# Kernel optimization log

Hardware: AMD Instinct MI355X
Metric: run time of the kernel (lower is better)

The kernel has to match this reference:

```python
import jax, jax.numpy as jnp
import numpy as np

NUM_WIRES = 4
N_LAYERS = 2
HIDDEN = 64
NUM_CLASSES = 10
B = 4096


def _ry(state, theta, wire):
    # state: (N,2,2,2,2); theta: scalar or (N,)
    st = jnp.moveaxis(state, wire + 1, 1)
    c = jnp.reshape(jnp.cos(theta / 2), (-1, 1, 1, 1))
    s = jnp.reshape(jnp.sin(theta / 2), (-1, 1, 1, 1))
    n0 = c * st[:, 0] - s * st[:, 1]
    n1 = s * st[:, 0] + c * st[:, 1]
    st = jnp.stack([n0, n1], axis=1)
    return jnp.moveaxis(st, 1, wire + 1)


def _cnot(state, ctrl, tgt):
    st = jnp.moveaxis(state, (ctrl + 1, tgt + 1), (1, 2))  # (N,2,2,2,2)
    st = jnp.stack([st[:, 0], st[:, 1, ::-1]], axis=1)
    return jnp.moveaxis(st, (1, 2), (ctrl + 1, tgt + 1))


def _zexp(state, wire):
    p = state * state  # real statevector -> probabilities
    axes = tuple(a for a in range(1, 5) if a != wire + 1)
    marg = p.sum(axes)  # (N,2)
    return marg[:, 0] - marg[:, 1]


def quantum_layer(angles, vparams):
    # angles: (N,4) data rotation angles; vparams: (2,4)
    N = angles.shape[0]
    state = jnp.zeros((N, 2, 2, 2, 2), angles.dtype).at[:, 0, 0, 0, 0].set(1.0)
    for w in range(NUM_WIRES):
        state = _ry(state, angles[:, w], w)
    for l in range(N_LAYERS):
        for w in range(NUM_WIRES):
            state = _ry(state, vparams[l, w], w)
        state = _cnot(state, 0, 1)
        state = _cnot(state, 1, 2)
        state = _cnot(state, 2, 3)
    return jnp.stack([_zexp(state, w) for w in range(NUM_WIRES)], axis=1)  # (N,4)


def setup_inputs() -> dict:
    key = jax.random.key(0)
    ks = jax.random.split(key, 8)
    x = jax.random.uniform(ks[0], (B, 28, 28), dtype=jnp.float32)
    vparams = jax.random.normal(ks[1], (N_LAYERS, NUM_WIRES), dtype=jnp.float32)
    w1 = jax.random.normal(ks[2], (HIDDEN, NUM_WIRES), dtype=jnp.float32) * 0.5
    b1 = jnp.zeros((HIDDEN,), jnp.float32)
    w2 = jax.random.normal(ks[3], (1, HIDDEN), dtype=jnp.float32) * 0.125
    b2 = jnp.zeros((1,), jnp.float32)
    W = jax.random.normal(ks[4], (NUM_CLASSES, NUM_WIRES * 14 * 14), dtype=jnp.float32) * 0.03
    b = jnp.zeros((NUM_CLASSES,), jnp.float32)
    return {"x": x, "vparams": vparams, "w1": w1, "b1": b1, "w2": w2, "b2": b2, "W": W, "b": b}


def reference(x, vparams, w1, b1, w2, b2, W, b):
    Bx = x.shape[0]
    # 2x2 stride-2 patches, order [(r,c),(r,c+1),(r+1,c),(r+1,c+1)], patches row-major
    patches = x.reshape(Bx, 14, 2, 14, 2).transpose(0, 1, 3, 2, 4).reshape(Bx, 196, 4)
    meas = quantum_layer(patches.reshape(-1, 4), vparams).reshape(Bx, 196, 4)
    h = jax.nn.relu(jnp.einsum('bpn,hn->bph', meas, w1) + b1)
    scores = (jnp.einsum('bph,oh->bpo', h, w2) + b2)[..., 0]  # (B,196)
    attn = jax.nn.softmax(scores, axis=1)[..., None]
    weighted = meas * attn
    flat = weighted.reshape(Bx, -1)  # (B,784)
    logits = flat @ W.T + b
    return jax.nn.log_softmax(logits, axis=-1)
```

## Files before the change

kernel.cpp:

```cpp
#include <hip/hip_runtime.h>
#include <math.h>

#define NP 196
#define NC 10

template<int CTRL>
__device__ __forceinline__ float dpp_sum_step(float x) {
    int t = __builtin_amdgcn_update_dpp(0, __float_as_int(x), CTRL, 0xf, 0xf, false);
    return x + __int_as_float(t);
}
__device__ __forceinline__ float row16_sum(float x) {
    x = dpp_sum_step<0x111>(x);
    x = dpp_sum_step<0x112>(x);
    x = dpp_sum_step<0x114>(x);
    x = dpp_sum_step<0x118>(x);
    return x;
}
__device__ __forceinline__ float bcast_lane(float x, int lane) {
    return __int_as_float(__builtin_amdgcn_readlane(__float_as_int(x), lane));
}

__global__ __launch_bounds__(256, 4) void quanv_fused(
    const float* __restrict__ x,
    const float* __restrict__ vparams,
    const float* __restrict__ w1,
    const float* __restrict__ b1,
    const float* __restrict__ w2,
    const float* __restrict__ b2,
    const float* __restrict__ W,
    const float* __restrict__ bias,
    float* __restrict__ out)
{
    __shared__ float s_part[11][16];

    const int tid  = threadIdx.x;
    const int b    = blockIdx.x;
    const int lane = tid & 63;
    const int wv   = tid >> 6;
    const int pt   = (tid < NP) ? tid : NP - 1;

    const int pr = pt / 14;
    const int pc = pt - pr * 14;
    const float* px = x + (size_t)b * 784 + (2 * pr) * 28 + 2 * pc;
    const float2 ra = *(const float2*)px;
    const float2 rb = *(const float2*)(px + 28);

    float cw[4], sw[4];
    __sincosf((ra.x + vparams[0]) * 0.5f, &sw[0], &cw[0]);
    __sincosf((ra.y + vparams[1]) * 0.5f, &sw[1], &cw[1]);
    __sincosf((rb.x + vparams[2]) * 0.5f, &sw[2], &cw[2]);
    __sincosf((rb.y + vparams[3]) * 0.5f, &sw[3], &cw[3]);

    float t[4] = {cw[0]*cw[1], cw[0]*sw[1], sw[0]*cw[1], sw[0]*sw[1]};
    float u[4] = {cw[2]*cw[3], cw[2]*sw[3], sw[2]*cw[3], sw[2]*sw[3]};
    float v[16];
    #pragma unroll
    for (int i = 0; i < 16; i++) v[i] = t[i >> 2] * u[i & 3];

    #pragma unroll
    for (int i = 0; i < 16; i++)
        if ((i & 8) && !(i & 4)) { const float tm = v[i]; v[i] = v[i | 4]; v[i | 4] = tm; }
    #pragma unroll
    for (int i = 0; i < 16; i++)
        if ((i & 4) && !(i & 2)) { const float tm = v[i]; v[i] = v[i | 2]; v[i | 2] = tm; }
    #pragma unroll
    for (int i = 0; i < 16; i++)
        if ((i & 2) && !(i & 1)) { const float tm = v[i]; v[i] = v[i | 1]; v[i | 1] = tm; }

    #pragma unroll
    for (int w = 0; w < 4; w++) {
        float c, s;
        __sincosf(vparams[4 + w] * 0.5f, &s, &c);
        const int m = 8 >> w;
        #pragma unroll
        for (int i = 0; i < 16; i++) {
            if ((i & m) == 0) {
                const float v0 = v[i], v1 = v[i | m];
                v[i]     = c * v0 - s * v1;
                v[i | m] = s * v0 + c * v1;
            }
        }
    }
    #pragma unroll
    for (int i = 0; i < 16; i++)
        if ((i & 8) && !(i & 4)) { const float tm = v[i]; v[i] = v[i | 4]; v[i | 4] = tm; }
    #pragma unroll
    for (int i = 0; i < 16; i++)
        if ((i & 4) && !(i & 2)) { const float tm = v[i]; v[i] = v[i | 2]; v[i | 2] = tm; }
    #pragma unroll
    for (int i = 0; i < 16; i++)
        if ((i & 2) && !(i & 1)) { const float tm = v[i]; v[i] = v[i | 1]; v[i | 1] = tm; }

    float p[16];
    #pragma unroll
    for (int i = 0; i < 16; i++) p[i] = v[i] * v[i];
    float e8[8], d8[8];
    #pragma unroll
    for (int j = 0; j < 8; j++) { e8[j] = p[2*j] + p[2*j+1]; d8[j] = p[2*j] - p[2*j+1]; }
    const float meas3 = ((d8[0]+d8[1]) + (d8[2]+d8[3])) + ((d8[4]+d8[5]) + (d8[6]+d8[7]));
    float f4[4], g4[4];
    #pragma unroll
    for (int k = 0; k < 4; k++) { f4[k] = e8[2*k] + e8[2*k+1]; g4[k] = e8[2*k] - e8[2*k+1]; }
    const float meas2 = (g4[0]+g4[1]) + (g4[2]+g4[3]);
    const float meas1 = (f4[0]-f4[1]) + (f4[2]-f4[3]);
    const float meas0 = (f4[0]+f4[1]) - (f4[2]+f4[3]);

    float sc0 = b2[0], sc1 = 0.f, sc2 = 0.f, sc3 = 0.f;
    #pragma unroll
    for (int j = 0; j < 64; j += 4) {
        float h0 = fmaf(w1[j*4 +  0], meas0, fmaf(w1[j*4 +  1], meas1,
                   fmaf(w1[j*4 +  2], meas2, fmaf(w1[j*4 +  3], meas3, b1[j]))));
        float h1 = fmaf(w1[j*4 +  4], meas0, fmaf(w1[j*4 +  5], meas1,
                   fmaf(w1[j*4 +  6], meas2, fmaf(w1[j*4 +  7], meas3, b1[j+1]))));
        float h2 = fmaf(w1[j*4 +  8], meas0, fmaf(w1[j*4 +  9], meas1,
                   fmaf(w1[j*4 + 10], meas2, fmaf(w1[j*4 + 11], meas3, b1[j+2]))));
        float h3 = fmaf(w1[j*4 + 12], meas0, fmaf(w1[j*4 + 13], meas1,
                   fmaf(w1[j*4 + 14], meas2, fmaf(w1[j*4 + 15], meas3, b1[j+3]))));
        sc0 = fmaf(w2[j],     fmaxf(h0, 0.f), sc0);
        sc1 = fmaf(w2[j + 1], fmaxf(h1, 0.f), sc1);
        sc2 = fmaf(w2[j + 2], fmaxf(h2, 0.f), sc2);
        sc3 = fmaf(w2[j + 3], fmaxf(h3, 0.f), sc3);
    }
    const float sc = (sc0 + sc1) + (sc2 + sc3);

    const float e = (tid < NP) ? __expf(sc) : 0.f;
    const float wm0 = e * meas0, wm1 = e * meas1;
    const float wm2 = e * meas2, wm3 = e * meas3;

    float r[11];
    #pragma unroll
    for (int o = 0; o < NC; o++) {
        const float4 Wv = *(const float4*)(W + o * 784 + pt * 4);
        r[o] = fmaf(wm0, Wv.x, fmaf(wm1, Wv.y, fmaf(wm2, Wv.z, wm3 * Wv.w)));
    }
    r[10] = e;

    #pragma unroll
    for (int i = 0; i < 11; i++) r[i] = row16_sum(r[i]);
    if ((lane & 15) == 15) {
        const int row = (wv << 2) | (lane >> 4);
        #pragma unroll
        for (int i = 0; i < 11; i++) s_part[i][row] = r[i];
    }
    __syncthreads();

    if (wv == 0) {
        float tot = 0.f;
        if (lane < 11) {
            const float4* q = (const float4*)s_part[lane];
            const float4 a = q[0], c = q[1], d = q[2], g = q[3];
            tot = (((a.x+a.y) + (a.z+a.w)) + ((c.x+c.y) + (c.z+c.w)))
                + (((d.x+d.y) + (d.z+d.w)) + ((g.x+g.y) + (g.z+g.w)));
        }
        const float esum = bcast_lane(tot, 10);
        const float rinv = __builtin_amdgcn_rcpf(esum);
        float logit = 0.f, ee = 0.f;
        if (lane < NC) {
            logit = fmaf(tot, rinv, bias[lane]);
            ee = __expf(logit);
        }
        const float ls = row16_sum(ee);
        const float lse = bcast_lane(ls, 15);
        if (lane < NC)
            out[(size_t)b * NC + lane] = logit - __logf(lse);
    }
}

extern "C" void kernel_launch(void* const* d_in, const int* in_sizes, int n_in,
                              void* d_out, int out_size, void* d_ws, size_t ws_size,
                              hipStream_t stream) {
    const float* x       = (const float*)d_in[0];
    const float* vparams = (const float*)d_in[1];
    const float* w1      = (const float*)d_in[2];
    const float* b1      = (const float*)d_in[3];
    const float* w2      = (const float*)d_in[4];
    const float* b2      = (const float*)d_in[5];
    const float* W       = (const float*)d_in[6];
    const float* bias    = (const float*)d_in[7];
    float* out           = (float*)d_out;

    const int B = in_sizes[0] / 784;
    quanv_fused<<<B, 256, 0, stream>>>(x, vparams, w1, b1, w2, b2, W, bias, out);
}
```

Before: 90.81 us.

## Map one image per wavefront with lanes looping over patches

Each wavefront now handles a whole image instead of each block handling one image with one patch per thread. Each lane simulates up to four patches in two passes, and the per-class reductions become pure wavefront DPP/readlane sums, so shared memory and the block barrier are gone. This also removes idle threads: 60 of 256 threads sat unused before, and now only the padded tail of the last pass is wasted. In exchange each lane does more serial work and holds more live registers, and W is reloaded per image per wave.

```diff
diff --git a/kernel.cpp b/kernel.cpp
--- a/kernel.cpp
+++ b/kernel.cpp
@@ -18,6 +18,98 @@
 }
 __device__ __forceinline__ float bcast_lane(float x, int lane) {
     return __int_as_float(__builtin_amdgcn_readlane(__float_as_int(x), lane));
+}
+__device__ __forceinline__ float wave_sum(float x) {
+    x = row16_sum(x);
+    x = dpp_sum_step<0x142>(x);
+    x = dpp_sum_step<0x143>(x);
+    return bcast_lane(x, 63);
+}
+
+__device__ __forceinline__ void patch_sim(
+    const float* __restrict__ xb, int p,
+    float vp0, float vp1, float vp2, float vp3,
+    const float* __restrict__ c1, const float* __restrict__ s1,
+    const float* __restrict__ w1, const float* __restrict__ b1,
+    const float* __restrict__ w2, float b2v,
+    float& m0, float& m1, float& m2, float& m3, float& sc)
+{
+    const int pr = p / 14;
+    const int pc = p - pr * 14;
+    const float* px = xb + (2 * pr) * 28 + 2 * pc;
+    const float2 ra = *(const float2*)px;
+    const float2 rb = *(const float2*)(px + 28);
+
+    float cw[4], sw[4];
+    __sincosf((ra.x + vp0) * 0.5f, &sw[0], &cw[0]);
+    __sincosf((ra.y + vp1) * 0.5f, &sw[1], &cw[1]);
+    __sincosf((rb.x + vp2) * 0.5f, &sw[2], &cw[2]);
+    __sincosf((rb.y + vp3) * 0.5f, &sw[3], &cw[3]);
+
+    float t[4] = {cw[0]*cw[1], cw[0]*sw[1], sw[0]*cw[1], sw[0]*sw[1]};
+    float u[4] = {cw[2]*cw[3], cw[2]*sw[3], sw[2]*cw[3], sw[2]*sw[3]};
+    float v[16];
+    #pragma unroll
+    for (int i = 0; i < 16; i++) v[i] = t[i >> 2] * u[i & 3];
+
+    #pragma unroll
+    for (int i = 0; i < 16; i++)
+        if ((i & 8) && !(i & 4)) { const float tm = v[i]; v[i] = v[i | 4]; v[i | 4] = tm; }
+    #pragma unroll
+    for (int i = 0; i < 16; i++)
+        if ((i & 4) && !(i & 2)) { const float tm = v[i]; v[i] = v[i | 2]; v[i | 2] = tm; }
+    #pragma unroll
+    for (int i = 0; i < 16; i++)
+        if ((i & 2) && !(i & 1)) { const float tm = v[i]; v[i] = v[i | 1]; v[i | 1] = tm; }
+
+    #pragma unroll
+    for (int w = 0; w < 4; w++) {
+        const float c = c1[w], s = s1[w];
+        const int m = 8 >> w;
+        #pragma unroll
+        for (int i = 0; i < 16; i++) {
+            if ((i & m) == 0) {
+                const float v0 = v[i], v1 = v[i | m];
+                v[i]     = c * v0 - s * v1;
+                v[i | m] = s * v0 + c * v1;
+            }
+        }
+    }
+    #pragma unroll
+    for (int i = 0; i < 16; i++)
+        if ((i & 8) && !(i & 4)) { const float tm = v[i]; v[i] = v[i | 4]; v[i | 4] = tm; }
+    #pragma unroll
+    for (int i = 0; i < 16; i++)
+        if ((i & 4) && !(i & 2)) { const float tm = v[i]; v[i] = v[i | 2]; v[i | 2] = tm; }
+    #pragma unroll
+    for (int i = 0; i < 16; i++)
+        if ((i & 2) && !(i & 1)) { const float tm = v[i]; v[i] = v[i | 1]; v[i | 1] = tm; }
+
+    float pp[16];
+    #pragma unroll
+    for (int i = 0; i < 16; i++) pp[i] = v[i] * v[i];
+    float e8[8], d8[8];
+    #pragma unroll
+    for (int j = 0; j < 8; j++) { e8[j] = pp[2*j] + pp[2*j+1]; d8[j] = pp[2*j] - pp[2*j+1]; }
+    m3 = ((d8[0]+d8[1]) + (d8[2]+d8[3])) + ((d8[4]+d8[5]) + (d8[6]+d8[7]));
+    float f4[4], g4[4];
+    #pragma unroll
+    for (int k = 0; k < 4; k++) { f4[k] = e8[2*k] + e8[2*k+1]; g4[k] = e8[2*k] - e8[2*k+1]; }
+    m2 = (g4[0]+g4[1]) + (g4[2]+g4[3]);
+    m1 = (f4[0]-f4[1]) + (f4[2]-f4[3]);
+    m0 = (f4[0]+f4[1]) - (f4[2]+f4[3]);
+
+    float sA = b2v, sB = 0.f;
+    #pragma unroll
+    for (int j = 0; j < 64; j += 2) {
+        float h0 = fmaf(w1[j*4 + 0], m0, fmaf(w1[j*4 + 1], m1,
+                   fmaf(w1[j*4 + 2], m2, fmaf(w1[j*4 + 3], m3, b1[j]))));
+        float h1 = fmaf(w1[j*4 + 4], m0, fmaf(w1[j*4 + 5], m1,
+                   fmaf(w1[j*4 + 6], m2, fmaf(w1[j*4 + 7], m3, b1[j+1]))));
+        sA = fmaf(w2[j],     fmaxf(h0, 0.f), sA);
+        sB = fmaf(w2[j + 1], fmaxf(h1, 0.f), sB);
+    }
+    sc = sA + sB;
 }
 
 __global__ __launch_bounds__(256, 4) void quanv_fused(
@@ -29,141 +121,73 @@
     const float* __restrict__ b2,
     const float* __restrict__ W,
     const float* __restrict__ bias,
-    float* __restrict__ out)
+    float* __restrict__ out,
+    int Btot)
 {
-    __shared__ float s_part[11][16];
-
     const int tid  = threadIdx.x;
-    const int b    = blockIdx.x;
     const int lane = tid & 63;
     const int wv   = tid >> 6;
-    const int pt   = (tid < NP) ? tid : NP - 1;
-
-    const int pr = pt / 14;
-    const int pc = pt - pr * 14;
-    const float* px = x + (size_t)b * 784 + (2 * pr) * 28 + 2 * pc;
-    const float2 ra = *(const float2*)px;
-    const float2 rb = *(const float2*)(px + 28);
-
-    float cw[4], sw[4];
-    __sincosf((ra.x + vparams[0]) * 0.5f, &sw[0], &cw[0]);
-    __sincosf((ra.y + vparams[1]) * 0.5f, &sw[1], &cw[1]);
-    __sincosf((rb.x + vparams[2]) * 0.5f, &sw[2], &cw[2]);
-    __sincosf((rb.y + vparams[3]) * 0.5f, &sw[3], &cw[3]);
-
-    float t[4] = {cw[0]*cw[1], cw[0]*sw[1], sw[0]*cw[1], sw[0]*sw[1]};
-    float u[4] = {cw[2]*cw[3], cw[2]*sw[3], sw[2]*cw[3], sw[2]*sw[3]};
-    float v[16];
-    #pragma unroll
-    for (int i = 0; i < 16; i++) v[i] = t[i >> 2] * u[i & 3];
-
-    #pragma unroll
-    for (int i = 0; i < 16; i++)
-        if ((i & 8) && !(i & 4)) { const float tm = v[i]; v[i] = v[i | 4]; v[i | 4] = tm; }
-    #pragma unroll
-    for (int i = 0; i < 16; i++)
-        if ((i & 4) && !(i & 2)) { const float tm = v[i]; v[i] = v[i | 2]; v[i | 2] = tm; }
-    #pragma unroll
-    for (int i = 0; i < 16; i++)
-        if ((i & 2) && !(i & 1)) { const float tm = v[i]; v[i] = v[i | 1]; v[i | 1] = tm; }
-
-    #pragma unroll
-    for (int w = 0; w < 4; w++) {
-        float c, s;
-        __sincosf(vparams[4 + w] * 0.5f, &s, &c);
-        const int m = 8 >> w;
+    const int img  = blockIdx.x * 4 + wv;
+    if (img >= Btot) return;
+    const float* xb = x + (size_t)img * 784;
+
+    const float vp0 = vparams[0], vp1 = vparams[1];
+    const float vp2 = vparams[2], vp3 = vparams[3];
+    float c1[4], s1[4];
+    #pragma unroll
+    for (int w = 0; w < 4; w++) __sincosf(vparams[4 + w] * 0.5f, &s1[w], &c1[w]);
+    const float b2v = b2[0];
+
+    float r[11];
+    #pragma unroll
+    for (int i = 0; i < 11; i++) r[i] = 0.f;
+
+    #pragma unroll
+    for (int pass = 0; pass < 2; pass++) {
+        const int pA = lane + pass * 128;
+        const int pB = pA + 64;
+        const bool vB = (pB < NP);
+        const int pBc = vB ? pB : NP - 1;
+
+        float a0, a1, a2, a3, scA;
+        float g0, g1, g2, g3, scB;
+        patch_sim(xb, pA,  vp0, vp1, vp2, vp3, c1, s1, w1, b1, w2, b2v, a0, a1, a2, a3, scA);
+        patch_sim(xb, pBc, vp0, vp1, vp2, vp3, c1, s1, w1, b1, w2, b2v, g0, g1, g2, g3, scB);
+
+        const float eA = __expf(scA);
+        const float eB = vB ? __expf(scB) : 0.f;
+        const float wA0 = eA * a0, wA1 = eA * a1, wA2 = eA * a2, wA3 = eA * a3;
+        const float wB0 = eB * g0, wB1 = eB * g1, wB2 = eB * g2, wB3 = eB * g3;
+
         #pragma unroll
-        for (int i = 0; i < 16; i++) {
-            if ((i & m) == 0) {
-                const float v0 = v[i], v1 = v[i | m];
-                v[i]     = c * v0 - s * v1;
-                v[i | m] = s * v0 + c * v1;
-            }
+        for (int o = 0; o < NC; o++) {
+            const float4 WA = *(const float4*)(W + o * 784 + pA  * 4);
+            const float4 WB = *(const float4*)(W + o * 784 + pBc * 4);
+            r[o] += fmaf(wA0, WA.x, fmaf(wA1, WA.y, fmaf(wA2, WA.z, wA3 * WA.w)))
+                  + fmaf(wB0, WB.x, fmaf(wB1, WB.y, fmaf(wB2, WB.z, wB3 * WB.w)));
         }
-    }
-    #pragma unroll
-    for (int i = 0; i < 16; i++)
-        if ((i & 8) && !(i & 4)) { const float tm = v[i]; v[i] = v[i | 4]; v[i | 4] = tm; }
-    #pragma unroll
-    for (int i = 0; i < 16; i++)
-        if ((i & 4) && !(i & 2)) { const float tm = v[i]; v[i] = v[i | 2]; v[i | 2] = tm; }
-    #pragma unroll
-    for (int i = 0; i < 16; i++)
-        if ((i & 2) && !(i & 1)) { const float tm = v[i]; v[i] = v[i | 1]; v[i | 1] = tm; }
-
-    float p[16];
-    #pragma unroll
-    for (int i = 0; i < 16; i++) p[i] = v[i] * v[i];
-    float e8[8], d8[8];
-    #pragma unroll
-    for (int j = 0; j < 8; j++) { e8[j] = p[2*j] + p[2*j+1]; d8[j] = p[2*j] - p[2*j+1]; }
-    const float meas3 = ((d8[0]+d8[1]) + (d8[2]+d8[3])) + ((d8[4]+d8[5]) + (d8[6]+d8[7]));
-    float f4[4], g4[4];
-    #pragma unroll
-    for (int k = 0; k < 4; k++) { f4[k] = e8[2*k] + e8[2*k+1]; g4[k] = e8[2*k] - e8[2*k+1]; }
-    const float meas2 = (g4[0]+g4[1]) + (g4[2]+g4[3]);
-    const float meas1 = (f4[0]-f4[1]) + (f4[2]-f4[3]);
-    const float meas0 = (f4[0]+f4[1]) - (f4[2]+f4[3]);
-
-    float sc0 = b2[0], sc1 = 0.f, sc2 = 0.f, sc3 = 0.f;
-    #pragma unroll
-    for (int j = 0; j < 64; j += 4) {
-        float h0 = fmaf(w1[j*4 +  0], meas0, fmaf(w1[j*4 +  1], meas1,
-                   fmaf(w1[j*4 +  2], meas2, fmaf(w1[j*4 +  3], meas3, b1[j]))));
-        float h1 = fmaf(w1[j*4 +  4], meas0, fmaf(w1[j*4 +  5], meas1,
-                   fmaf(w1[j*4 +  6], meas2, fmaf(w1[j*4 +  7], meas3, b1[j+1]))));
-        float h2 = fmaf(w1[j*4 +  8], meas0, fmaf(w1[j*4 +  9], meas1,
-                   fmaf(w1[j*4 + 10], meas2, fmaf(w1[j*4 + 11], meas3, b1[j+2]))));
-        float h3 = fmaf(w1[j*4 + 12], meas0, fmaf(w1[j*4 + 13], meas1,
-                   fmaf(w1[j*4 + 14], meas2, fmaf(w1[j*4 + 15], meas3, b1[j+3]))));
-        sc0 = fmaf(w2[j],     fmaxf(h0, 0.f), sc0);
-        sc1 = fmaf(w2[j + 1], fmaxf(h1, 0.f), sc1);
-        sc2 = fmaf(w2[j + 2], fmaxf(h2, 0.f), sc2);
-        sc3 = fmaf(w2[j + 3], fmaxf(h3, 0.f), sc3);
-    }
-    const float sc = (sc0 + sc1) + (sc2 + sc3);
-
-    const float e = (tid < NP) ? __expf(sc) : 0.f;
-    const float wm0 = e * meas0, wm1 = e * meas1;
-    const float wm2 = e * meas2, wm3 = e * meas3;
-
-    float r[11];
-    #pragma unroll
-    for (int o = 0; o < NC; o++) {
-        const float4 Wv = *(const float4*)(W + o * 784 + pt * 4);
-        r[o] = fmaf(wm0, Wv.x, fmaf(wm1, Wv.y, fmaf(wm2, Wv.z, wm3 * Wv.w)));
-    }
-    r[10] = e;
-
-    #pragma unroll
-    for (int i = 0; i < 11; i++) r[i] = row16_sum(r[i]);
-    if ((lane & 15) == 15) {
-        const int row = (wv << 2) | (lane >> 4);
-        #pragma unroll
-        for (int i = 0; i < 11; i++) s_part[i][row] = r[i];
-    }
-    __syncthreads();
-
-    if (wv == 0) {
-        float tot = 0.f;
-        if (lane < 11) {
-            const float4* q = (const float4*)s_part[lane];
-            const float4 a = q[0], c = q[1], d = q[2], g = q[3];
-            tot = (((a.x+a.y) + (a.z+a.w)) + ((c.x+c.y) + (c.z+c.w)))
-                + (((d.x+d.y) + (d.z+d.w)) + ((g.x+g.y) + (g.z+g.w)));
-        }
-        const float esum = bcast_lane(tot, 10);
-        const float rinv = __builtin_amdgcn_rcpf(esum);
-        float logit = 0.f, ee = 0.f;
-        if (lane < NC) {
-            logit = fmaf(tot, rinv, bias[lane]);
-            ee = __expf(logit);
-        }
-        const float ls = row16_sum(ee);
-        const float lse = bcast_lane(ls, 15);
-        if (lane < NC)
-            out[(size_t)b * NC + lane] = logit - __logf(lse);
-    }
+        r[10] += eA + eB;
+    }
+
+    float esum = 0.f;
+    float mytot = 0.f;
+    #pragma unroll
+    for (int i = 0; i < 11; i++) {
+        const float tv = wave_sum(r[i]);
+        if (i < NC) { if (lane == i) mytot = tv; }
+        else        esum = tv;
+    }
+
+    const float rinv = __builtin_amdgcn_rcpf(esum);
+    float logit = 0.f, ee = 0.f;
+    if (lane < NC) {
+        logit = fmaf(mytot, rinv, bias[lane]);
+        ee = __expf(logit);
+    }
+    const float ls  = row16_sum(ee);
+    const float lse = bcast_lane(ls, 15);
+    if (lane < NC)
+        out[(size_t)img * NC + lane] = logit - __logf(lse);
 }
 
 extern "C" void kernel_launch(void* const* d_in, const int* in_sizes, int n_in,
@@ -180,5 +204,5 @@
     float* out           = (float*)d_out;
 
     const int B = in_sizes[0] / 784;
-    quanv_fused<<<B, 256, 0, stream>>>(x, vparams, w1, b1, w2, b2, W, bias, out);
-}
+    quanv_fused<<<(B + 3) / 4, 256, 0, stream>>>(x, vparams, w1, b1, w2, b2, W, bias, out, B);
+}
```

Result: slower. 98.19 us (+8.1%).

## Split fused kernel into dense per-patch kernel and per-image reduction kernel

Applied to the files above, without the earlier changes.

The single fused kernel is split into two launches. The first maps one thread per patch across all images with no idle lanes and writes the attention-weighted measurements and exp scores to a workspace in structure-of-arrays form. The second kernel reads them back per image and does the W projection, reduction and log-softmax. This removes the 60 idle threads per 256-thread block in the heavy quantum/MLP stage. In exchange it adds a global-memory round trip of about 16 MB and a second kernel launch.

```diff
diff --git a/kernel.cpp b/kernel.cpp
--- a/kernel.cpp
+++ b/kernel.cpp
@@ -20,28 +20,24 @@
     return __int_as_float(__builtin_amdgcn_readlane(__float_as_int(x), lane));
 }
 
-__global__ __launch_bounds__(256, 4) void quanv_fused(
+__global__ __launch_bounds__(256) void k_patch(
     const float* __restrict__ x,
     const float* __restrict__ vparams,
     const float* __restrict__ w1,
     const float* __restrict__ b1,
     const float* __restrict__ w2,
     const float* __restrict__ b2,
-    const float* __restrict__ W,
-    const float* __restrict__ bias,
-    float* __restrict__ out)
+    float* __restrict__ ws,
+    int total)
 {
-    __shared__ float s_part[11][16];
-
-    const int tid  = threadIdx.x;
-    const int b    = blockIdx.x;
-    const int lane = tid & 63;
-    const int wv   = tid >> 6;
-    const int pt   = (tid < NP) ? tid : NP - 1;
-
-    const int pr = pt / 14;
-    const int pc = pt - pr * 14;
-    const float* px = x + (size_t)b * 784 + (2 * pr) * 28 + 2 * pc;
+    const int g = blockIdx.x * 256 + threadIdx.x;
+    if (g >= total) return;
+    const int img = g / NP;
+    const int p   = g - img * NP;
+
+    const int pr = p / 14;
+    const int pc = p - pr * 14;
+    const float* px = x + (size_t)img * 784 + (2 * pr) * 28 + 2 * pc;
     const float2 ra = *(const float2*)px;
     const float2 rb = *(const float2*)(px + 28);
 
@@ -91,31 +87,31 @@
     for (int i = 0; i < 16; i++)
         if ((i & 2) && !(i & 1)) { const float tm = v[i]; v[i] = v[i | 1]; v[i | 1] = tm; }
 
-    float p[16];
-    #pragma unroll
-    for (int i = 0; i < 16; i++) p[i] = v[i] * v[i];
+    float pp[16];
+    #pragma unroll
+    for (int i = 0; i < 16; i++) pp[i] = v[i] * v[i];
     float e8[8], d8[8];
     #pragma unroll
-    for (int j = 0; j < 8; j++) { e8[j] = p[2*j] + p[2*j+1]; d8[j] = p[2*j] - p[2*j+1]; }
-    const float meas3 = ((d8[0]+d8[1]) + (d8[2]+d8[3])) + ((d8[4]+d8[5]) + (d8[6]+d8[7]));
+    for (int j = 0; j < 8; j++) { e8[j] = pp[2*j] + pp[2*j+1]; d8[j] = pp[2*j] - pp[2*j+1]; }
+    const float m3v = ((d8[0]+d8[1]) + (d8[2]+d8[3])) + ((d8[4]+d8[5]) + (d8[6]+d8[7]));
     float f4[4], g4[4];
     #pragma unroll
     for (int k = 0; k < 4; k++) { f4[k] = e8[2*k] + e8[2*k+1]; g4[k] = e8[2*k] - e8[2*k+1]; }
-    const float meas2 = (g4[0]+g4[1]) + (g4[2]+g4[3]);
-    const float meas1 = (f4[0]-f4[1]) + (f4[2]-f4[3]);
-    const float meas0 = (f4[0]+f4[1]) - (f4[2]+f4[3]);
+    const float m2v = (g4[0]+g4[1]) + (g4[2]+g4[3]);
+    const float m1v = (f4[0]-f4[1]) + (f4[2]-f4[3]);
+    const float m0v = (f4[0]+f4[1]) - (f4[2]+f4[3]);
 
     float sc0 = b2[0], sc1 = 0.f, sc2 = 0.f, sc3 = 0.f;
     #pragma unroll
     for (int j = 0; j < 64; j += 4) {
-        float h0 = fmaf(w1[j*4 +  0], meas0, fmaf(w1[j*4 +  1], meas1,
-                   fmaf(w1[j*4 +  2], meas2, fmaf(w1[j*4 +  3], meas3, b1[j]))));
-        float h1 = fmaf(w1[j*4 +  4], meas0, fmaf(w1[j*4 +  5], meas1,
-                   fmaf(w1[j*4 +  6], meas2, fmaf(w1[j*4 +  7], meas3, b1[j+1]))));
-        float h2 = fmaf(w1[j*4 +  8], meas0, fmaf(w1[j*4 +  9], meas1,
-                   fmaf(w1[j*4 + 10], meas2, fmaf(w1[j*4 + 11], meas3, b1[j+2]))));
-        float h3 = fmaf(w1[j*4 + 12], meas0, fmaf(w1[j*4 + 13], meas1,
-                   fmaf(w1[j*4 + 14], meas2, fmaf(w1[j*4 + 15], meas3, b1[j+3]))));
+        float h0 = fmaf(w1[j*4 +  0], m0v, fmaf(w1[j*4 +  1], m1v,
+                   fmaf(w1[j*4 +  2], m2v, fmaf(w1[j*4 +  3], m3v, b1[j]))));
+        float h1 = fmaf(w1[j*4 +  4], m0v, fmaf(w1[j*4 +  5], m1v,
+                   fmaf(w1[j*4 +  6], m2v, fmaf(w1[j*4 +  7], m3v, b1[j+1]))));
+        float h2 = fmaf(w1[j*4 +  8], m0v, fmaf(w1[j*4 +  9], m1v,
+                   fmaf(w1[j*4 + 10], m2v, fmaf(w1[j*4 + 11], m3v, b1[j+2]))));
+        float h3 = fmaf(w1[j*4 + 12], m0v, fmaf(w1[j*4 + 13], m1v,
+                   fmaf(w1[j*4 + 14], m2v, fmaf(w1[j*4 + 15], m3v, b1[j+3]))));
         sc0 = fmaf(w2[j],     fmaxf(h0, 0.f), sc0);
         sc1 = fmaf(w2[j + 1], fmaxf(h1, 0.f), sc1);
         sc2 = fmaf(w2[j + 2], fmaxf(h2, 0.f), sc2);
@@ -123,9 +119,36 @@
     }
     const float sc = (sc0 + sc1) + (sc2 + sc3);
 
-    const float e = (tid < NP) ? __expf(sc) : 0.f;
-    const float wm0 = e * meas0, wm1 = e * meas1;
-    const float wm2 = e * meas2, wm3 = e * meas3;
+    const float e = __expf(sc);
+    ws[0 * (size_t)total + g] = e * m0v;
+    ws[1 * (size_t)total + g] = e * m1v;
+    ws[2 * (size_t)total + g] = e * m2v;
+    ws[3 * (size_t)total + g] = e * m3v;
+    ws[4 * (size_t)total + g] = e;
+}
+
+__global__ __launch_bounds__(256, 4) void k_reduce(
+    const float* __restrict__ ws,
+    const float* __restrict__ W,
+    const float* __restrict__ bias,
+    float* __restrict__ out,
+    int total)
+{
+    __shared__ float s_part[11][16];
+
+    const int tid  = threadIdx.x;
+    const int b    = blockIdx.x;
+    const int lane = tid & 63;
+    const int wv   = tid >> 6;
+    const int pt   = (tid < NP) ? tid : NP - 1;
+    const float sel = (tid < NP) ? 1.f : 0.f;
+    const size_t base = (size_t)b * NP + pt;
+
+    const float wm0 = sel * ws[0 * (size_t)total + base];
+    const float wm1 = sel * ws[1 * (size_t)total + base];
+    const float wm2 = sel * ws[2 * (size_t)total + base];
+    const float wm3 = sel * ws[3 * (size_t)total + base];
+    const float e   = sel * ws[4 * (size_t)total + base];
 
     float r[11];
     #pragma unroll
@@ -159,7 +182,7 @@
             logit = fmaf(tot, rinv, bias[lane]);
             ee = __expf(logit);
         }
-        const float ls = row16_sum(ee);
+        const float ls  = row16_sum(ee);
         const float lse = bcast_lane(ls, 15);
         if (lane < NC)
             out[(size_t)b * NC + lane] = logit - __logf(lse);
@@ -178,7 +201,11 @@
     const float* W       = (const float*)d_in[6];
     const float* bias    = (const float*)d_in[7];
     float* out           = (float*)d_out;
+    float* ws            = (float*)d_ws;
 
     const int B = in_sizes[0] / 784;
-    quanv_fused<<<B, 256, 0, stream>>>(x, vparams, w1, b1, w2, b2, W, bias, out);
-}
+    const int total = B * NP;
+
+    k_patch<<<(total + 255) / 256, 256, 0, stream>>>(x, vparams, w1, b1, w2, b2, ws, total);
+    k_reduce<<<B, 256, 0, stream>>>(ws, W, bias, out, total);
+}
```

Result: slower. 95.62 us (+5.3%).
